# Kernel tuning notes

Measured on AMD Instinct MI355X. Metric: run time of the kernel, lower is better.

## Reference

```python
import jax, jax.numpy as jnp
import numpy as np

B, T, N, F, H = 64, 50, 24, 256, 256  # batch, timesteps, graph nodes, input feat, hidden


def setup_inputs() -> dict:
    key = jax.random.key(0)
    ks = jax.random.split(key, 12)
    sF = 1.0 / np.sqrt(F)
    sH = 1.0 / np.sqrt(H)
    u = lambda k, shape, s: jax.random.uniform(k, shape, jnp.float32, -s, s)
    return {
        "x": jax.random.normal(ks[0], (B, T, N, F), jnp.float32),
        "G": jax.random.normal(ks[1], (N, N), jnp.float32) / np.sqrt(N),
        "W_ih": u(ks[2], (4 * H, F), sF),
        "b_ih": u(ks[3], (4 * H,), sF),
        "W_hh": u(ks[4], (4 * H, H), sH),
        "b_hh": u(ks[5], (4 * H,), sH),
        "W_h1": u(ks[6], (H, F), sF),
        "b_h1": u(ks[7], (H,), sF),
        "W_h2": u(ks[8], (H, F), sF),
        "b_h2": u(ks[9], (H,), sF),
        "W_fc": u(ks[10], (H, H), sH),
        "b_fc": u(ks[11], (H,), sH),
    }


def graph_linear(G, x, W, b):
    # GraphLinear: node-mixing G then feature projection W, bias after mixing
    # x: [B, N, f_in] -> [B, N, f_out]
    return jnp.einsum('nm,bmf->bnf', G, x @ W.T) + b


def reference(x, G, W_ih, b_ih, W_hh, b_hh, W_h1, b_h1, W_h2, b_h2, W_fc, b_fc):
    x0 = x[:, 0]                                   # [B, N, F]
    h = graph_linear(G, x0, W_h1, b_h1)            # initial hidden
    c = graph_linear(G, x0, W_h2, b_h2)            # initial cell

    def step(carry, xt):
        h, c = carry
        gates = (graph_linear(G, xt, W_ih, b_ih)
                 + graph_linear(G, h, W_hh, b_hh))  # [B, N, 4H]
        i, f, g, o = jnp.split(gates, 4, axis=-1)
        c = jax.nn.sigmoid(f) * c + jax.nn.sigmoid(i) * jnp.tanh(g)
        h = jax.nn.sigmoid(o) * jnp.tanh(c)
        return (h, c), None

    (h, c), _ = jax.lax.scan(step, (h, c), jnp.swapaxes(x, 0, 1))  # scan over T
    # dropout(p=0.0) is identity; final projection + tanh on last timestep output
    return jnp.tanh(graph_linear(G, h, W_fc, b_fc))
```

## Files before the change

kernel.cpp:

```cpp
#include <hip/hip_runtime.h>
#include <stdint.h>

#define T_ 50

typedef float f32x4 __attribute__((ext_vector_type(4)));
typedef short s16x8 __attribute__((ext_vector_type(8)));

#define WS_WIH   0u
#define WS_WHH   524288u
#define WS_WINIT 1048576u
#define WS_WFC   1310720u
#define WS_GPAD  1441792u
#define WS_FLG   1443840u
#define WS_NEED  1460224u

#define L_WHH  0
#define L_A1   131072
#define L_A2   143360
#define L_ZR   155648
#define L_HST  156160
#define L_HST2 160256
#define L_TOT  163328

__device__ __forceinline__ f32x4 mfma16(s16x8 a, s16x8 b, f32x4 c){
  return __builtin_amdgcn_mfma_f32_16x16x32_bf16(a, b, c, 0, 0, 0);
}
__device__ __forceinline__ uint32_t bfbits(float f){
  uint32_t u = __builtin_bit_cast(uint32_t, f);
  u += 0x7FFFu + ((u >> 16) & 1u);
  return u >> 16;
}
__device__ __forceinline__ uint32_t pk2bf(float lo, float hi){
  return bfbits(lo) | (bfbits(hi) << 16);
}
#define LOG2E 1.4426950408889634f
__device__ __forceinline__ float fexp2(float x){ return __builtin_amdgcn_exp2f(x); }
__device__ __forceinline__ float frcp_(float x){ return __builtin_amdgcn_rcpf(x); }
__device__ __forceinline__ float fsig(float x){ return frcp_(1.f + fexp2(-LOG2E * x)); }
__device__ __forceinline__ float ftanh_(float x){ return 1.f - 2.f * frcp_(1.f + fexp2(2.f * LOG2E * x)); }

__global__ void prep_kernel(const float* __restrict__ G,
                            const float* __restrict__ Wih, const float* __restrict__ Whh,
                            const float* __restrict__ Wh1, const float* __restrict__ Wh2,
                            const float* __restrict__ Wfc, uint8_t* __restrict__ ws)
{
  const int tid = blockIdx.x * blockDim.x + threadIdx.x;
  const int nth = gridDim.x * blockDim.x;
  uint16_t* wih = (uint16_t*)(ws + WS_WIH);
  uint16_t* whh = (uint16_t*)(ws + WS_WHH);
  uint16_t* wini= (uint16_t*)(ws + WS_WINIT);
  uint16_t* wfc = (uint16_t*)(ws + WS_WFC);
  uint16_t* gp  = (uint16_t*)(ws + WS_GPAD);
  uint32_t* flg = (uint32_t*)(ws + WS_FLG);

  for (int i = tid; i < 262144; i += nth){
    int cg = i >> 16, c = (i >> 8) & 255, k = i & 255;
    int row = (c >> 6)*256 + 64*cg + (c & 63);
    wih[i] = (uint16_t)bfbits(Wih[row*256 + k]);
    whh[i] = (uint16_t)bfbits(Whh[row*256 + k]);
  }
  for (int i = tid; i < 131072; i += nth){
    int cg = i >> 15, c = (i >> 8) & 127, k = i & 255;
    float v = (c < 64) ? Wh1[(64*cg + c)*256 + k] : Wh2[(64*cg + c - 64)*256 + k];
    wini[i] = (uint16_t)bfbits(v);
  }
  for (int i = tid; i < 65536; i += nth){
    int cg = i >> 14, c = (i >> 8) & 63, k = i & 255;
    wfc[i] = (uint16_t)bfbits(Wfc[(64*cg + c)*256 + k]);
  }
  for (int i = tid; i < 1024; i += nth){
    int n = i >> 5, m = i & 31;
    gp[i] = (n < 24 && m < 24) ? (uint16_t)bfbits(G[n*24 + m]) : (uint16_t)0;
  }
  for (int i = tid; i < 4096; i += nth) flg[i] = 0;
}

__global__ void __launch_bounds__(512, 1)
encoder_kernel(const float* __restrict__ x, uint8_t* __restrict__ ws,
               float* __restrict__ out,
               const float* __restrict__ bih, const float* __restrict__ bhh,
               const float* __restrict__ bh1, const float* __restrict__ bh2,
               const float* __restrict__ bfc)
{
  extern __shared__ uint8_t smem[];
  uint16_t* WHHL = (uint16_t*)(smem + L_WHH);
  uint16_t* A1   = (uint16_t*)(smem + L_A1);
  uint16_t* A2   = (uint16_t*)(smem + L_A2);
  uint16_t* ZR   = (uint16_t*)(smem + L_ZR);
  uint16_t* HST  = (uint16_t*)(smem + L_HST);
  uint16_t* HST2 = (uint16_t*)(smem + L_HST2);

  const int tid = threadIdx.x;
  const int b   = blockIdx.x & 63;
  const int cg  = blockIdx.x >> 6;
  const int w   = tid >> 6;
  const int l   = tid & 63;
  const int l15 = l & 15;
  const int g   = l >> 4;
  const int Mt  = w >> 2;
  const int ns  = w & 3;
  const int ul  = ns*16 + l15;
  const int ug  = 64*cg + ul;

  const uint16_t* WIH  = (const uint16_t*)(ws + WS_WIH)   + (size_t)cg*65536;
  const uint16_t* WINI = (const uint16_t*)(ws + WS_WINIT) + (size_t)cg*32768;
  const uint16_t* WFC  = (const uint16_t*)(ws + WS_WFC)   + (size_t)cg*16384;
  const uint16_t* GP   = (const uint16_t*)(ws + WS_GPAD);
  uint32_t* flgB = (uint32_t*)(ws + WS_FLG) + b*64;
  uint32_t* flgW = flgB + cg*16;
  uint16_t* GhB  = (uint16_t*)((uint8_t*)out + (size_t)b*24576);

  {
    const uint8_t* src = ws + WS_WHH + (size_t)cg*131072;
    for (int i = tid*8; i < 65536; i += 4096){
      uint4 v = *(const uint4*)(src + (size_t)i*2);
      int col = i >> 8, k0 = i & 255;
      *(uint4*)&WHHL[col*256 + (k0 ^ ((col&7)<<3))] = v;
    }
  }
  for (int i = tid; i < 256;  i += 512) ZR[i] = 0;
  for (int i = tid; i < 2048; i += 512) HST[i] = 0;

  s16x8 gfragM = *(const s16x8*)&GP[(Mt*16 + l15)*32 + g*8];

  const float bb0 = bih[ug]     + bhh[ug];
  const float bb1 = bih[256+ug] + bhh[256+ug];
  const float bb2 = bih[512+ug] + bhh[512+ug];
  const float bb3 = bih[768+ug] + bhh[768+ug];
  const float bh1l = bh1[ug], bh2l = bh2[ug], bfcl = bfc[ug];

  const int arow = Mt*16 + l15;
  const uint16_t* a1row = (arow < 24) ? (A1 + arow*256) : ZR;
  const uint16_t* a2row = (arow < 24) ? (A2 + arow*256) : ZR;
  const int sw = (arow < 24) ? ((arow & 7) << 3) : 0;

  auto gx_stage = [&](const float* xt){
    #pragma unroll
    for (int jt = 0; jt < 4; jt++){
      int f = (jt*4 + ns)*16 + l15;
      s16x8 bfrag = (s16x8){0,0,0,0,0,0,0,0};
      if (g < 3){
        uint4 q;
        q.x = pk2bf(xt[(g*8+0)*256+f], xt[(g*8+1)*256+f]);
        q.y = pk2bf(xt[(g*8+2)*256+f], xt[(g*8+3)*256+f]);
        q.z = pk2bf(xt[(g*8+4)*256+f], xt[(g*8+5)*256+f]);
        q.w = pk2bf(xt[(g*8+6)*256+f], xt[(g*8+7)*256+f]);
        bfrag = __builtin_bit_cast(s16x8, q);
      }
      f32x4 zz = {0.f,0.f,0.f,0.f};
      f32x4 gx = mfma16(gfragM, bfrag, zz);
      int n0 = Mt*16 + g*4;
      if (n0 < 24){
        uint32_t a01 = pk2bf(gx[0], gx[1]), a23 = pk2bf(gx[2], gx[3]);
        A2[(n0  )*256 + (f ^ (((n0  )&7)<<3))] = (uint16_t)a01;
        A2[(n0+1)*256 + (f ^ (((n0+1)&7)<<3))] = (uint16_t)(a01>>16);
        A2[(n0+2)*256 + (f ^ (((n0+2)&7)<<3))] = (uint16_t)a23;
        A2[(n0+3)*256 + (f ^ (((n0+3)&7)<<3))] = (uint16_t)(a23>>16);
      }
    }
  };

  auto stageA1 = [&](int parity){
    const unsigned long long* gs = (const unsigned long long*)(GhB + parity*6144);
    unsigned long long v0 = __hip_atomic_load(gs + tid,        __ATOMIC_RELAXED, __HIP_MEMORY_SCOPE_AGENT);
    unsigned long long v1 = __hip_atomic_load(gs + tid + 512,  __ATOMIC_RELAXED, __HIP_MEMORY_SCOPE_AGENT);
    unsigned long long v2 = __hip_atomic_load(gs + tid + 1024, __ATOMIC_RELAXED, __HIP_MEMORY_SCOPE_AGENT);
    int k0 = (tid & 63) << 2;
    int n0 = tid >> 6, n1 = n0 + 8, n2 = n0 + 16;
    *(unsigned long long*)&A1[n0*256 + (k0 ^ ((n0&7)<<3))] = v0;
    *(unsigned long long*)&A1[n1*256 + (k0 ^ ((n1&7)<<3))] = v1;
    *(unsigned long long*)&A1[n2*256 + (k0 ^ ((n2&7)<<3))] = v2;
  };

  auto wait_for = [&](uint32_t target){
    if (tid < 4){
      uint32_t* fp = flgB + tid*16;
      int guard = 0;
      while (__hip_atomic_load(fp, __ATOMIC_RELAXED, __HIP_MEMORY_SCOPE_AGENT) < target){
        __builtin_amdgcn_s_sleep(1);
        if (++guard > 20000000) break;
      }
    }
    __syncthreads();
  };

  auto do_publish = [&](const float hv[4], int parity, uint32_t flagval){
    int n0 = Mt*16 + g*4;
    if (n0 < 24){
      uint2 p; p.x = pk2bf(hv[0], hv[1]); p.y = pk2bf(hv[2], hv[3]);
      *(uint2*)&HST[ul*32 + n0] = p;
    }
    __syncthreads();
    s16x8 hb = *(const s16x8*)&HST[ul*32 + g*8];
    f32x4 zz = {0.f,0.f,0.f,0.f};
    f32x4 gh = mfma16(gfragM, hb, zz);
    if (n0 < 24){
      uint32_t q01 = pk2bf(gh[0], gh[1]), q23 = pk2bf(gh[2], gh[3]);
      HST2[(n0  )*64 + ul] = (uint16_t)q01;
      HST2[(n0+1)*64 + ul] = (uint16_t)(q01>>16);
      HST2[(n0+2)*64 + ul] = (uint16_t)q23;
      HST2[(n0+3)*64 + ul] = (uint16_t)(q23>>16);
    }
    __syncthreads();
    if (tid < 384){
      int node = tid >> 4, c4 = tid & 15;
      unsigned long long v = *(const unsigned long long*)&HST2[node*64 + c4*4];
      __hip_atomic_store((unsigned long long*)(GhB + parity*6144) + node*64 + cg*16 + c4,
                         v, __ATOMIC_RELAXED, __HIP_MEMORY_SCOPE_AGENT);
    }
    asm volatile("s_waitcnt vmcnt(0)" ::: "memory");
    __syncthreads();
    if (tid == 0)
      __hip_atomic_store(flgW, flagval, __ATOMIC_RELAXED, __HIP_MEMORY_SCOPE_AGENT);
  };

  float cst[4];
  f32x4 zacc[4];

  gx_stage(x + (size_t)b*T_*6144);
  __syncthreads();
  {
    f32x4 h0a = {0.f,0.f,0.f,0.f}, c0a = {0.f,0.f,0.f,0.f};
    #pragma unroll
    for (int j = 0; j < 4; j++) zacc[j] = (f32x4){0.f,0.f,0.f,0.f};
    #pragma unroll
    for (int ks = 0; ks < 8; ks++){
      const int kk = ks*32 + g*8;
      s16x8 a  = *(const s16x8*)&a2row[kk ^ sw];
      s16x8 b1 = *(const s16x8*)&WINI[ul*256 + kk];
      s16x8 b2 = *(const s16x8*)&WINI[(64+ul)*256 + kk];
      h0a = mfma16(a, b1, h0a);
      c0a = mfma16(a, b2, c0a);
      #pragma unroll
      for (int j = 0; j < 4; j++){
        s16x8 bz = *(const s16x8*)&WIH[((j*4+ns)*16 + l15)*256 + kk];
        zacc[j] = mfma16(a, bz, zacc[j]);
      }
    }
    float hv0[4];
    #pragma unroll
    for (int r = 0; r < 4; r++){
      cst[r] = c0a[r] + bh2l;
      hv0[r] = h0a[r] + bh1l;
    }
    do_publish(hv0, 1, 1u);
  }
  gx_stage(x + ((size_t)b*T_ + 1)*6144);

  for (int t = 0; t < T_; t++){
    wait_for((uint32_t)(t+1));
    stageA1((t+1)&1);
    __syncthreads();

    f32x4 uacc[4];
    #pragma unroll
    for (int j = 0; j < 4; j++) uacc[j] = zacc[j];
    #pragma unroll
    for (int ks = 0; ks < 8; ks++){
      const int kk = ks*32 + g*8;
      s16x8 a = *(const s16x8*)&a1row[kk ^ sw];
      #pragma unroll
      for (int j = 0; j < 4; j++){
        int col = (j*4+ns)*16 + l15;
        s16x8 bf = *(const s16x8*)&WHHL[col*256 + (kk ^ ((col&7)<<3))];
        uacc[j] = mfma16(a, bf, uacc[j]);
      }
    }
    float hv[4];
    #pragma unroll
    for (int r = 0; r < 4; r++){
      float ig = fsig  (uacc[0][r] + bb0);
      float fg = fsig  (uacc[1][r] + bb1);
      float gg = ftanh_(uacc[2][r] + bb2);
      float og = fsig  (uacc[3][r] + bb3);
      float c  = fg*cst[r] + ig*gg;
      cst[r] = c;
      hv[r] = og*ftanh_(c);
    }
    do_publish(hv, t & 1, (uint32_t)(t+2));

    if (t+1 < T_){
      #pragma unroll
      for (int j = 0; j < 4; j++) zacc[j] = (f32x4){0.f,0.f,0.f,0.f};
      #pragma unroll
      for (int ks = 0; ks < 8; ks++){
        const int kk = ks*32 + g*8;
        s16x8 a = *(const s16x8*)&a2row[kk ^ sw];
        #pragma unroll
        for (int j = 0; j < 4; j++){
          s16x8 bf = *(const s16x8*)&WIH[((j*4+ns)*16 + l15)*256 + kk];
          zacc[j] = mfma16(a, bf, zacc[j]);
        }
      }
    }
    __syncthreads();
    if (t+1 < T_){
      int tn = (t+2 < T_) ? (t+2) : (T_-1);
      gx_stage(x + ((size_t)b*T_ + tn)*6144);
    }
  }

  wait_for((uint32_t)(T_+1));
  stageA1(1);
  __syncthreads();
  if (tid == 0)
    __hip_atomic_store(flgW, (uint32_t)(T_+2), __ATOMIC_RELAXED, __HIP_MEMORY_SCOPE_AGENT);
  wait_for((uint32_t)(T_+2));
  {
    f32x4 oacc = {0.f,0.f,0.f,0.f};
    #pragma unroll
    for (int ks = 0; ks < 8; ks++){
      const int kk = ks*32 + g*8;
      s16x8 a  = *(const s16x8*)&a1row[kk ^ sw];
      s16x8 bf = *(const s16x8*)&WFC[ul*256 + kk];
      oacc = mfma16(a, bf, oacc);
    }
    int n0 = Mt*16 + g*4;
    if (n0 < 24){
      #pragma unroll
      for (int r = 0; r < 4; r++)
        out[(size_t)b*6144 + (n0+r)*256 + ug] = ftanh_(oacc[r] + bfcl);
    }
  }
}

extern "C" void kernel_launch(void* const* d_in, const int* in_sizes, int n_in,
                              void* d_out, int out_size, void* d_ws, size_t ws_size,
                              hipStream_t stream)
{
  (void)in_sizes; (void)n_in; (void)out_size;
  if (ws_size < WS_NEED) return;

  const float* x   = (const float*)d_in[0];
  const float* G   = (const float*)d_in[1];
  const float* Wih = (const float*)d_in[2];
  const float* bih = (const float*)d_in[3];
  const float* Whh = (const float*)d_in[4];
  const float* bhh = (const float*)d_in[5];
  const float* Wh1 = (const float*)d_in[6];
  const float* bh1 = (const float*)d_in[7];
  const float* Wh2 = (const float*)d_in[8];
  const float* bh2 = (const float*)d_in[9];
  const float* Wfc = (const float*)d_in[10];
  const float* bfc = (const float*)d_in[11];
  uint8_t* ws = (uint8_t*)d_ws;
  float* outp = (float*)d_out;

  hipLaunchKernelGGL(prep_kernel, dim3(256), dim3(256), 0, stream,
                     G, Wih, Whh, Wh1, Wh2, Wfc, ws);

  hipFuncSetAttribute((const void*)encoder_kernel,
                      hipFuncAttributeMaxDynamicSharedMemorySize, L_TOT);
  void* args[] = {(void*)&x, (void*)&ws, (void*)&outp,
                  (void*)&bih, (void*)&bhh, (void*)&bh1, (void*)&bh2, (void*)&bfc};
  hipLaunchCooperativeKernel((const void*)encoder_kernel, dim3(256), dim3(512),
                             args, L_TOT, stream);
}
```

Baseline: 642.4 us.

## Load published hidden state straight into MFMA fragments and prefetch x via LDS

The shared hidden state is now read from global memory directly into per-lane A-operand registers, which removes the LDS A1 staging buffer and one barrier on the recurrent critical path. The next timestep's x tile is loaded with coalesced 16-byte vector loads issued early, before the input-projection MFMAs, then converted to bf16 and written to a padded LDS buffer that gx_stage reads from. This replaces strided scalar global loads and hides their latency behind compute. In exchange, each lane issues more redundant global atomic loads of the hidden state, and the x path adds extra barriers and LDS traffic.

Result: slower. 677.8 us (+5.5%).

```diff
diff --git a/kernel.cpp b/kernel.cpp
--- a/kernel.cpp
+++ b/kernel.cpp
@@ -5,6 +5,7 @@
 
 typedef float f32x4 __attribute__((ext_vector_type(4)));
 typedef short s16x8 __attribute__((ext_vector_type(8)));
+typedef uint64_t u64x2 __attribute__((ext_vector_type(2)));
 
 #define WS_WIH   0u
 #define WS_WHH   524288u
@@ -15,12 +16,12 @@
 #define WS_NEED  1460224u
 
 #define L_WHH  0
-#define L_A1   131072
-#define L_A2   143360
-#define L_ZR   155648
-#define L_HST  156160
-#define L_HST2 160256
-#define L_TOT  163328
+#define L_A2   131072
+#define L_XL   143360
+#define L_ZR   155840
+#define L_HST  156352
+#define L_HST2 160448
+#define L_TOT  163520
 
 __device__ __forceinline__ f32x4 mfma16(s16x8 a, s16x8 b, f32x4 c){
   return __builtin_amdgcn_mfma_f32_16x16x32_bf16(a, b, c, 0, 0, 0);
@@ -84,8 +85,8 @@
 {
   extern __shared__ uint8_t smem[];
   uint16_t* WHHL = (uint16_t*)(smem + L_WHH);
-  uint16_t* A1   = (uint16_t*)(smem + L_A1);
   uint16_t* A2   = (uint16_t*)(smem + L_A2);
+  uint16_t* XL   = (uint16_t*)(smem + L_XL);
   uint16_t* ZR   = (uint16_t*)(smem + L_ZR);
   uint16_t* HST  = (uint16_t*)(smem + L_HST);
   uint16_t* HST2 = (uint16_t*)(smem + L_HST2);
@@ -130,22 +131,34 @@
   const float bh1l = bh1[ug], bh2l = bh2[ug], bfcl = bfc[ug];
 
   const int arow = Mt*16 + l15;
-  const uint16_t* a1row = (arow < 24) ? (A1 + arow*256) : ZR;
+  const int crow = (arow < 24) ? arow : 23;
   const uint16_t* a2row = (arow < 24) ? (A2 + arow*256) : ZR;
   const int sw = (arow < 24) ? ((arow & 7) << 3) : 0;
 
-  auto gx_stage = [&](const float* xt){
+  auto xld_issue = [&](const float* xt, f32x4 xv[3]){
+    #pragma unroll
+    for (int p = 0; p < 3; p++)
+      xv[p] = *(const f32x4*)(xt + tid*4 + p*2048);
+  };
+  auto xld_write = [&](const f32x4 xv[3]){
+    #pragma unroll
+    for (int p = 0; p < 3; p++){
+      int e = tid*4 + p*2048;
+      int m = e >> 8, f = e & 255;
+      uint2 pk; pk.x = pk2bf(xv[p][0], xv[p][1]); pk.y = pk2bf(xv[p][2], xv[p][3]);
+      *(uint2*)&XL[m*260 + f] = pk;
+    }
+  };
+
+  auto gx_stage = [&](){
     #pragma unroll
     for (int jt = 0; jt < 4; jt++){
       int f = (jt*4 + ns)*16 + l15;
       s16x8 bfrag = (s16x8){0,0,0,0,0,0,0,0};
       if (g < 3){
-        uint4 q;
-        q.x = pk2bf(xt[(g*8+0)*256+f], xt[(g*8+1)*256+f]);
-        q.y = pk2bf(xt[(g*8+2)*256+f], xt[(g*8+3)*256+f]);
-        q.z = pk2bf(xt[(g*8+4)*256+f], xt[(g*8+5)*256+f]);
-        q.w = pk2bf(xt[(g*8+6)*256+f], xt[(g*8+7)*256+f]);
-        bfrag = __builtin_bit_cast(s16x8, q);
+        #pragma unroll
+        for (int j = 0; j < 8; j++)
+          bfrag[j] = (short)XL[(g*8 + j)*260 + f];
       }
       f32x4 zz = {0.f,0.f,0.f,0.f};
       f32x4 gx = mfma16(gfragM, bfrag, zz);
@@ -160,16 +173,14 @@
     }
   };
 
-  auto stageA1 = [&](int parity){
+  auto ghload = [&](int parity, unsigned long long af[8][2]){
     const unsigned long long* gs = (const unsigned long long*)(GhB + parity*6144);
-    unsigned long long v0 = __hip_atomic_load(gs + tid,        __ATOMIC_RELAXED, __HIP_MEMORY_SCOPE_AGENT);
-    unsigned long long v1 = __hip_atomic_load(gs + tid + 512,  __ATOMIC_RELAXED, __HIP_MEMORY_SCOPE_AGENT);
-    unsigned long long v2 = __hip_atomic_load(gs + tid + 1024, __ATOMIC_RELAXED, __HIP_MEMORY_SCOPE_AGENT);
-    int k0 = (tid & 63) << 2;
-    int n0 = tid >> 6, n1 = n0 + 8, n2 = n0 + 16;
-    *(unsigned long long*)&A1[n0*256 + (k0 ^ ((n0&7)<<3))] = v0;
-    *(unsigned long long*)&A1[n1*256 + (k0 ^ ((n1&7)<<3))] = v1;
-    *(unsigned long long*)&A1[n2*256 + (k0 ^ ((n2&7)<<3))] = v2;
+    #pragma unroll
+    for (int ks = 0; ks < 8; ks++){
+      int e = crow*64 + ks*8 + g*2;
+      af[ks][0] = __hip_atomic_load(gs + e,     __ATOMIC_RELAXED, __HIP_MEMORY_SCOPE_AGENT);
+      af[ks][1] = __hip_atomic_load(gs + e + 1, __ATOMIC_RELAXED, __HIP_MEMORY_SCOPE_AGENT);
+    }
   };
 
   auto wait_for = [&](uint32_t target){
@@ -216,8 +227,15 @@
 
   float cst[4];
   f32x4 zacc[4];
-
-  gx_stage(x + (size_t)b*T_*6144);
+  const float* xb = x + (size_t)b*T_*6144;
+
+  {
+    f32x4 xv[3];
+    xld_issue(xb, xv);
+    xld_write(xv);
+  }
+  __syncthreads();
+  gx_stage();
   __syncthreads();
   {
     f32x4 h0a = {0.f,0.f,0.f,0.f}, c0a = {0.f,0.f,0.f,0.f};
@@ -245,12 +263,18 @@
     }
     do_publish(hv0, 1, 1u);
   }
-  gx_stage(x + ((size_t)b*T_ + 1)*6144);
+  {
+    f32x4 xv[3];
+    xld_issue(xb + 6144, xv);
+    xld_write(xv);
+    __syncthreads();
+    gx_stage();
+  }
 
   for (int t = 0; t < T_; t++){
     wait_for((uint32_t)(t+1));
-    stageA1((t+1)&1);
-    __syncthreads();
+    unsigned long long af[8][2];
+    ghload((t+1)&1, af);
 
     f32x4 uacc[4];
     #pragma unroll
@@ -258,7 +282,8 @@
     #pragma unroll
     for (int ks = 0; ks < 8; ks++){
       const int kk = ks*32 + g*8;
-      s16x8 a = *(const s16x8*)&a1row[kk ^ sw];
+      u64x2 q; q.x = af[ks][0]; q.y = af[ks][1];
+      s16x8 a = __builtin_bit_cast(s16x8, q);
       #pragma unroll
       for (int j = 0; j < 4; j++){
         int col = (j*4+ns)*16 + l15;
@@ -280,6 +305,9 @@
     do_publish(hv, t & 1, (uint32_t)(t+2));
 
     if (t+1 < T_){
+      int tn = (t+2 < T_) ? (t+2) : (T_-1);
+      f32x4 xv[3];
+      xld_issue(xb + (size_t)tn*6144, xv);
       #pragma unroll
       for (int j = 0; j < 4; j++) zacc[j] = (f32x4){0.f,0.f,0.f,0.f};
       #pragma unroll
@@ -292,16 +320,17 @@
           zacc[j] = mfma16(a, bf, zacc[j]);
         }
       }
-    }
-    __syncthreads();
-    if (t+1 < T_){
-      int tn = (t+2 < T_) ? (t+2) : (T_-1);
-      gx_stage(x + ((size_t)b*T_ + tn)*6144);
+      __syncthreads();
+      xld_write(xv);
+      __syncthreads();
+      gx_stage();
     }
   }
 
   wait_for((uint32_t)(T_+1));
-  stageA1(1);
+  unsigned long long af[8][2];
+  ghload(1, af);
+  asm volatile("s_waitcnt vmcnt(0)" ::: "memory");
   __syncthreads();
   if (tid == 0)
     __hip_atomic_store(flgW, (uint32_t)(T_+2), __ATOMIC_RELAXED, __HIP_MEMORY_SCOPE_AGENT);
@@ -311,7 +340,8 @@
     #pragma unroll
     for (int ks = 0; ks < 8; ks++){
       const int kk = ks*32 + g*8;
-      s16x8 a  = *(const s16x8*)&a1row[kk ^ sw];
+      u64x2 q; q.x = af[ks][0]; q.y = af[ks][1];
+      s16x8 a  = __builtin_bit_cast(s16x8, q);
       s16x8 bf = *(const s16x8*)&WFC[ul*256 + kk];
       oacc = mfma16(a, bf, oacc);
     }
```
